# Kernel tuning notes

Hardware: AMD Instinct MI355X
Metric: run time of the kernel (lower is better)

Reference implementation:

```python
import jax, jax.numpy as jnp
import numpy as np

V, E, H = 100000, 300, 256          # pretrained vectors, emb_dim, rep_dim
B, QLEN, DOC, S = 32, 32, 2048, 64  # batch, max_query_len, max_doc_len, max_num_sent
L = DOC // S                        # sentence length (lengths sum exactly to DOC)
VOCAB = V + 2                       # + extra token + padding idx


def _uniform(k, shape, scale):
    return jax.random.uniform(k, shape, jnp.float32, -scale, scale)


def setup_inputs() -> dict:
    key = jax.random.key(0)
    ks = jax.random.split(key, 16)
    s = 1.0 / np.sqrt(H)  # PyTorch GRU default init scale
    return {
        "queries": jax.random.randint(ks[0], (B, QLEN), 0, V),
        "query_lengths": jax.random.randint(ks[1], (B,), QLEN // 2, QLEN + 1).astype(jnp.int32),
        "docs": jax.random.randint(ks[2], (B, DOC), 0, V),
        "sentence_lengths": jnp.full((B, S), L, dtype=jnp.int32),
        "emb": jax.random.normal(ks[3], (VOCAB, E), jnp.float32) * 0.1,
        "q_wih": _uniform(ks[4], (3 * H, E), s), "q_whh": _uniform(ks[5], (3 * H, H), s),
        "q_bih": _uniform(ks[6], (3 * H,), s), "q_bhh": _uniform(ks[7], (3 * H,), s),
        "f_wih": _uniform(ks[8], (3 * H, E), s), "f_whh": _uniform(ks[9], (3 * H, H), s),
        "f_bih": _uniform(ks[10], (3 * H,), s), "f_bhh": _uniform(ks[11], (3 * H,), s),
        "b_wih": _uniform(ks[12], (3 * H, E), s), "b_whh": _uniform(ks[13], (3 * H, H), s),
        "b_bih": _uniform(ks[14], (3 * H,), s), "b_bhh": _uniform(ks[15], (3 * H,), s),
    }


def _gru(x, wih, whh, bih, bhh, reverse=False):
    # x: (B, T, E) -> hidden states (B, T, H); PyTorch GRU cell equations.
    xg = jnp.einsum('bte,ge->btg', x, wih) + bih  # (B, T, 3H) input projections

    def step(h, xt):
        gh = h @ whh.T + bhh
        ir, iz, inn = jnp.split(xt, 3, axis=-1)
        hr, hz, hn = jnp.split(gh, 3, axis=-1)
        r = jax.nn.sigmoid(ir + hr)
        z = jax.nn.sigmoid(iz + hz)
        n = jnp.tanh(inn + r * hn)
        hnew = (1.0 - z) * n + z * h
        return hnew, hnew

    h0 = jnp.zeros((x.shape[0], whh.shape[1]), x.dtype)
    _, hs = jax.lax.scan(step, h0, jnp.swapaxes(xg, 0, 1), reverse=reverse)
    return jnp.swapaxes(hs, 0, 1)


def reference(queries, query_lengths, docs, sentence_lengths, emb,
              q_wih, q_whh, q_bih, q_bhh,
              f_wih, f_whh, f_bih, f_bhh,
              b_wih, b_whh, b_bih, b_bhh):
    q_emb = emb[queries]  # (B, QLEN, E)
    d_emb = emb[docs]     # (B, DOC, E)

    # Ragged per-sentence mean pooling (_get_facts) as one segment-mean per doc.
    def seg_mean(xb, lens):
        ids = jnp.repeat(jnp.arange(S), lens, total_repeat_length=DOC)
        sums = jax.ops.segment_sum(xb, ids, num_segments=S)
        return sums / jnp.maximum(lens, 1)[:, None].astype(xb.dtype)

    facts = jax.vmap(seg_mean)(d_emb, sentence_lengths)  # (B, S, E)

    # Question GRU: hidden state at the last valid token (pack_padded semantics).
    q_hs = _gru(q_emb, q_wih, q_whh, q_bih, q_bhh)
    q_rep = q_hs[jnp.arange(B), query_lengths - 1][:, None, :]  # (B, 1, H)

    # Input fusion: bidirectional GRU over facts, fwd + bwd halves summed (dropout off / eval).
    f_out = (_gru(facts, f_wih, f_whh, f_bih, f_bhh)
             + _gru(facts, b_wih, b_whh, b_bih, b_bhh, reverse=True))  # (B, S, H)

    num_facts = jnp.sum(sentence_lengths > 0, axis=1)
    return q_rep, f_out, num_facts
```

## Files before the change

### kernel.cpp

```cpp
#include <hip/hip_runtime.h>

#define Bn   32
#define QL   32
#define DOCn 2048
#define Sn   64
#define En   300
#define Hn   256

typedef short bf16x8 __attribute__((ext_vector_type(8)));
typedef short s16x4  __attribute__((ext_vector_type(4)));
typedef float f32x4  __attribute__((ext_vector_type(4)));

static __device__ __forceinline__ float b2f(short s){
  unsigned int u = ((unsigned int)(unsigned short)s) << 16;
  float f; __builtin_memcpy(&f, &u, 4); return f;
}
static __device__ __forceinline__ short f2b(float f){
  unsigned int u; __builtin_memcpy(&u, &f, 4);
  u = u + 0x7fffu + ((u >> 16) & 1u);
  return (short)(u >> 16);
}
static __device__ __forceinline__ float sigm(float x){ return 1.0f/(1.0f+__expf(-x)); }
static __device__ __forceinline__ float tanhx(float x){ return 1.0f - 2.0f/(__expf(2.0f*x)+1.0f); }
static __device__ __forceinline__ f32x4 mfma16(bf16x8 a, bf16x8 b, f32x4 c){
  return __builtin_amdgcn_mfma_f32_16x16x32_bf16(a, b, c, 0, 0, 0);
}
static __device__ __forceinline__ void bar_lgkm(){
  asm volatile("s_waitcnt lgkmcnt(0)\n\ts_barrier" ::: "memory");
}

__global__ __launch_bounds__(256) void k_facts(
    const int* __restrict__ docs, const int* __restrict__ slens,
    const float* __restrict__ emb,
    const float* __restrict__ f_wih, const float* __restrict__ b_wih,
    const float* __restrict__ q_wih,
    short* __restrict__ facts, short* __restrict__ wcvt,
    float* __restrict__ dout)
{
  const int tid = threadIdx.x;

  if (blockIdx.x >= 2048){
    const int rg0 = (blockIdx.x - 2048)*8;
#pragma unroll
    for (int rr = 0; rr < 8; ++rr){
      const int rg = rg0 + rr;
      const int z = rg / 768, g = rg % 768;
      const float* src = ((z == 0) ? f_wih : (z == 1) ? b_wih : q_wih) + (long)g*En;
      short* dst = wcvt + (long)rg*320;
      for (int c = tid; c < 320; c += 256)
        dst[c] = (c < En) ? f2b(src[c]) : (short)0;
    }
    return;
  }

  __shared__ int pref[2*Sn];
  const int blk = blockIdx.x;
  const int b = blk >> 6, s = blk & 63;
  if (tid < Sn){
    const int v = slens[b*Sn + tid];
    int x = v;
#pragma unroll
    for (int d = 1; d < 64; d <<= 1){
      const int y = __shfl_up(x, d, 64);
      if (tid >= d) x += y;
    }
    pref[tid] = x - v;
    pref[Sn + tid] = v;
    if (s == 0){
      const unsigned long long m = __ballot(v > 0);
      if (tid == 0) dout[Bn*Hn + (long)Bn*Sn*Hn + b] = (float)__popcll(m);
    }
  }
  __syncthreads();
  const int off = pref[s];
  const int len = pref[Sn + s];
  const int e0 = tid;
  float a0 = 0.f, a1 = 0.f;
  const int* dtok = docs + b*DOCn + off;
  int tk = (len > 0) ? dtok[0] : 0;
  for (int l = 0; l < len; ++l){
    const int tkn = (l + 1 < len) ? dtok[l+1] : 0;
    const float* row = emb + (long)tk*En;
    a0 += row[e0];
    if (e0 + 256 < En) a1 += row[e0+256];
    tk = tkn;
  }
  const float inv = 1.0f / (float)(len > 0 ? len : 1);
  short* frow = facts + ((long)b*Sn + s)*320;
  frow[e0] = f2b(a0*inv);
  if (e0 < 64) frow[e0+256] = (e0 + 256 < En) ? f2b(a1*inv) : (short)0;
}

__global__ __launch_bounds__(256) void k_xg(
    const short* __restrict__ facts, const short* __restrict__ wcvt,
    const int* __restrict__ queries, const float* __restrict__ emb,
    const float* __restrict__ q_bih, const float* __restrict__ q_bhh,
    const float* __restrict__ f_bih, const float* __restrict__ f_bhh,
    const float* __restrict__ b_bih, const float* __restrict__ b_bhh,
    short* __restrict__ q_xgi, short* __restrict__ f_xgi,
    short* __restrict__ b_xgi)
{
  const int z = blockIdx.z;
  const int bm = blockIdx.x, bn = blockIdx.y;
  const bool isq = (z == 2);
  if (isq && bm >= 8) return;

  const float* bih = (z == 0) ? f_bih : (z == 1) ? b_bih : q_bih;
  const float* bhh = (z == 0) ? f_bhh : (z == 1) ? b_bhh : q_bhh;
  short*       xgi = (z == 0) ? f_xgi : (z == 1) ? b_xgi : q_xgi;

  __shared__ alignas(16) short Al[2][128][40];
  const int tid = threadIdx.x;
  const int l = tid & 63, w = tid >> 6;
  const int wm = w & 1, wn = w >> 1;
  const int l15 = l & 15, lq = l >> 4;
  const int ak8 = w*8;

  bf16x8 bfr[2][10];
#pragma unroll
  for (int nt = 0; nt < 2; ++nt){
    const int g = bn*64 + wn*32 + nt*16 + l15;
    const short* wr = wcvt + ((long)z*768 + g)*320;
#pragma unroll
    for (int kk = 0; kk < 10; ++kk)
      bfr[nt][kk] = *(const bf16x8*)&wr[kk*32 + lq*8];
  }

  const short* asrc_f0 = nullptr; const short* asrc_f1 = nullptr;
  const float* asrc_q0 = nullptr; const float* asrc_q1 = nullptr;
  if (isq){
    asrc_q0 = emb + (long)queries[bm*128 + l]*En;
    asrc_q1 = emb + (long)queries[bm*128 + 64 + l]*En;
  } else {
    asrc_f0 = facts + (long)(bm*128 + l)*320;
    asrc_f1 = facts + (long)(bm*128 + 64 + l)*320;
  }

  bf16x8 va0, va1;
#define LDA_(KK) do{ const int k0_ = (KK)*32 + ak8; \
    if (!isq){ \
      va0 = *(const bf16x8*)(asrc_f0 + k0_); \
      va1 = *(const bf16x8*)(asrc_f1 + k0_); \
    } else if (k0_ + 7 < En){ \
      const f32x4 p0 = *(const f32x4*)(asrc_q0+k0_), p1 = *(const f32x4*)(asrc_q0+k0_+4); \
      const f32x4 p2 = *(const f32x4*)(asrc_q1+k0_), p3 = *(const f32x4*)(asrc_q1+k0_+4); \
      _Pragma("unroll") for (int j = 0; j < 4; ++j){ \
        va0[j] = f2b(p0[j]); va0[4+j] = f2b(p1[j]); \
        va1[j] = f2b(p2[j]); va1[4+j] = f2b(p3[j]); } \
    } else { \
      _Pragma("unroll") for (int j = 0; j < 8; ++j){ const int k_ = k0_ + j; \
        va0[j] = (k_ < En) ? f2b(asrc_q0[k_]) : (short)0; \
        va1[j] = (k_ < En) ? f2b(asrc_q1[k_]) : (short)0; } \
    } }while(0)
#define STA_(BUF) do{ *(bf16x8*)&Al[BUF][l][ak8] = va0; \
    *(bf16x8*)&Al[BUF][64 + l][ak8] = va1; }while(0)

  LDA_(0); STA_(0);
  __syncthreads();

  f32x4 acc[4][2] = {};
#pragma unroll
  for (int kk = 0; kk < 10; ++kk){
    if (kk < 9) LDA_(kk+1);
#pragma unroll
    for (int mt = 0; mt < 4; ++mt){
      bf16x8 a = *(const bf16x8*)&Al[kk&1][wm*64 + mt*16 + l15][lq*8];
      acc[mt][0] = mfma16(a, bfr[0][kk], acc[mt][0]);
      acc[mt][1] = mfma16(a, bfr[1][kk], acc[mt][1]);
    }
    if (kk < 9) STA_((kk+1)&1);
    __syncthreads();
  }
#undef LDA_
#undef STA_

#pragma unroll
  for (int nt = 0; nt < 2; ++nt){
    const int cg = bn*64 + wn*32 + nt*16 + l15;
    float bias = bih[cg];
    if (cg < 512) bias += bhh[cg];
    const int gate = cg >> 8, hc = cg & 255;
#pragma unroll
    for (int mt = 0; mt < 4; ++mt){
      const int r0 = bm*128 + wm*64 + mt*16 + lq*4;
#pragma unroll
      for (int p = 0; p < 4; ++p){
        const int r = r0 + p;
        const int row = isq ? ((r & 31)*32 + (r >> 5)) : ((r & 63)*32 + (r >> 6));
        xgi[(long)row*1024 + hc*4 + gate] = f2b(acc[mt][nt][p] + bias);
      }
    }
  }
}

__global__ __launch_bounds__(1024) void k_gru(
    const short* __restrict__ q_xg, const short* __restrict__ f_xg,
    const short* __restrict__ b_xg,
    const float* __restrict__ q_whh, const float* __restrict__ q_bhh,
    const float* __restrict__ f_whh, const float* __restrict__ f_bhh,
    const float* __restrict__ b_whh, const float* __restrict__ b_bhh,
    const int* __restrict__ qlens,
    float* __restrict__ dout)
{
  __shared__ alignas(16) short hl[2*16*264];
  __shared__ alignas(16) short wl[7*1024*8];

  const int gru = blockIdx.x >> 1;
  const int mh  = blockIdx.x & 1;
  const int tid = threadIdx.x;
  const int l = tid & 63, w = tid >> 6;
  const int l15 = l & 15, lq = l >> 4;

  const float* whh = (gru == 0) ? q_whh : (gru == 1) ? f_whh : b_whh;
  const float* bhh = (gru == 0) ? q_bhh : (gru == 1) ? f_bhh : b_bhh;
  const short* xgp = (gru == 0) ? q_xg  : (gru == 1) ? f_xg  : b_xg;
  const int T = (gru == 0) ? QL : Sn;

  const int c = w*16 + l15;

  bf16x8 wf[3][6];
  float bhn = 0.f;
#pragma unroll
  for (int gi = 0; gi < 3; ++gi){
    const int g = gi*256 + c;
    const float* wr = whh + (long)g*Hn;
#pragma unroll
    for (int kk = 0; kk < 8; ++kk){
      const f32x4 f0 = *(const f32x4*)(wr + kk*32 + lq*8);
      const f32x4 f1 = *(const f32x4*)(wr + kk*32 + lq*8 + 4);
      bf16x8 v;
#pragma unroll
      for (int j = 0; j < 4; ++j){ v[j] = f2b(f0[j]); v[4+j] = f2b(f1[j]); }
      if (kk < 5 || (kk == 5 && gi < 2)) wf[gi][kk] = v;
      else if (kk == 5)                  *(bf16x8*)&wl[(6*1024 + tid)*8] = v;
      else                               *(bf16x8*)&wl[(((kk-6)*3 + gi)*1024 + tid)*8] = v;
    }
    if (gi == 2) bhn = bhh[g];
  }

  float hreg[4] = {};
  int qlen_m[4];
#pragma unroll
  for (int p = 0; p < 4; ++p) qlen_m[p] = (gru == 0) ? qlens[mh*16 + lq*4 + p] : -1;

  const int vo = (mh*16 + lq*4)*1024 + c*4;
  float* qdst  = dout + (mh*16 + lq*4)*Hn + c;
  float* fbase = dout + Bn*Hn + (long)(mh*16 + lq*4)*(Sn*Hn) + c;

  s16x4 preA[4], preB[4];

#define TOF(TT) ((gru == 2) ? (T - 1 - (TT)) : (TT))
#define LOADP(PRE, TI) do{ const short* sb_ = xgp + (long)(TI)*32768 + vo; \
    PRE[0] = *(const s16x4*)(sb_); \
    PRE[1] = *(const s16x4*)(sb_ + 1024); \
    PRE[2] = *(const s16x4*)(sb_ + 2048); \
    PRE[3] = *(const s16x4*)(sb_ + 3072); }while(0)

#define GRU_STEP(TT, DOM, HIN, HOUT, PRE) do{ \
    f32x4 acc0 = (f32x4){0.f,0.f,0.f,0.f}; \
    f32x4 acc1 = (f32x4){0.f,0.f,0.f,0.f}; \
    f32x4 acc2 = (f32x4){bhn,bhn,bhn,bhn}; \
    if (DOM){ \
      _Pragma("unroll") for (int kk = 0; kk < 5; ++kk){ \
        const bf16x8 a = *(const bf16x8*)&(HIN)[l15*264 + kk*32 + lq*8]; \
        acc0 = mfma16(a, wf[0][kk], acc0); \
        acc1 = mfma16(a, wf[1][kk], acc1); \
        acc2 = mfma16(a, wf[2][kk], acc2); \
      } \
      { const bf16x8 a = *(const bf16x8*)&(HIN)[l15*264 + 5*32 + lq*8]; \
        const bf16x8 w2 = *(const bf16x8*)&wl[(6*1024 + tid)*8]; \
        acc0 = mfma16(a, wf[0][5], acc0); \
        acc1 = mfma16(a, wf[1][5], acc1); \
        acc2 = mfma16(a, w2, acc2); } \
      { const bf16x8 a = *(const bf16x8*)&(HIN)[l15*264 + 6*32 + lq*8]; \
        const bf16x8 w0 = *(const bf16x8*)&wl[(0*1024 + tid)*8]; \
        const bf16x8 w1 = *(const bf16x8*)&wl[(1*1024 + tid)*8]; \
        const bf16x8 w2 = *(const bf16x8*)&wl[(2*1024 + tid)*8]; \
        acc0 = mfma16(a, w0, acc0); \
        acc1 = mfma16(a, w1, acc1); \
        acc2 = mfma16(a, w2, acc2); } \
      { const bf16x8 a = *(const bf16x8*)&(HIN)[l15*264 + 7*32 + lq*8]; \
        const bf16x8 w0 = *(const bf16x8*)&wl[(3*1024 + tid)*8]; \
        const bf16x8 w1 = *(const bf16x8*)&wl[(4*1024 + tid)*8]; \
        const bf16x8 w2 = *(const bf16x8*)&wl[(5*1024 + tid)*8]; \
        acc0 = mfma16(a, w0, acc0); \
        acc1 = mfma16(a, w1, acc1); \
        acc2 = mfma16(a, w2, acc2); } \
    } \
    const int t_ = TOF(TT); \
    _Pragma("unroll") for (int p = 0; p < 4; ++p){ \
      const float ir = b2f(PRE[p][0]), iz = b2f(PRE[p][1]), in_ = b2f(PRE[p][2]); \
      const float rr = sigm(ir + acc0[p]); \
      const float zz = sigm(iz + acc1[p]); \
      const float nn = tanhx(in_ + rr*acc2[p]); \
      const float hn = (1.0f - zz)*nn + zz*hreg[p]; \
      hreg[p] = hn; \
      (HOUT)[(lq*4 + p)*264 + c] = f2b(hn); \
      if (gru == 0){ if (t_ == qlen_m[p] - 1) qdst[p*Hn] = hn; } \
      else { atomicAdd(fbase + p*(Sn*Hn) + t_*Hn, hn); } \
    } \
  }while(0)

  short* h0 = hl;
  short* h1 = hl + 4224;

  LOADP(preA, TOF(0));
  LOADP(preB, TOF(1));
  __builtin_amdgcn_sched_barrier(0);
  GRU_STEP(0, 0, h1, h0, preA);
  bar_lgkm();
  LOADP(preA, TOF(2));
  __builtin_amdgcn_sched_barrier(0);
  GRU_STEP(1, 1, h0, h1, preB);
  bar_lgkm();

  for (int tt = 2; tt < T; tt += 2){
    const int tiB = (tt+1 < T) ? (tt+1) : (T-1);
    LOADP(preB, TOF(tiB));
    __builtin_amdgcn_sched_barrier(0);
    GRU_STEP(tt, 1, h1, h0, preA);
    bar_lgkm();
    const int tiA = (tt+2 < T) ? (tt+2) : (T-1);
    LOADP(preA, TOF(tiA));
    __builtin_amdgcn_sched_barrier(0);
    GRU_STEP(tt+1, 1, h0, h1, preB);
    bar_lgkm();
  }
#undef TOF
#undef LOADP
#undef GRU_STEP
}

extern "C" void kernel_launch(void* const* d_in, const int* in_sizes, int n_in,
                              void* d_out, int out_size, void* d_ws, size_t ws_size,
                              hipStream_t stream)
{
  const int*   queries = (const int*)d_in[0];
  const int*   qlens   = (const int*)d_in[1];
  const int*   docs    = (const int*)d_in[2];
  const int*   slens   = (const int*)d_in[3];
  const float* emb     = (const float*)d_in[4];
  const float* q_wih   = (const float*)d_in[5];
  const float* q_whh   = (const float*)d_in[6];
  const float* q_bih   = (const float*)d_in[7];
  const float* q_bhh   = (const float*)d_in[8];
  const float* f_wih   = (const float*)d_in[9];
  const float* f_whh   = (const float*)d_in[10];
  const float* f_bih   = (const float*)d_in[11];
  const float* f_bhh   = (const float*)d_in[12];
  const float* b_wih   = (const float*)d_in[13];
  const float* b_whh   = (const float*)d_in[14];
  const float* b_bih   = (const float*)d_in[15];
  const float* b_bhh   = (const float*)d_in[16];

  char* wsb = (char*)d_ws;
  short* f_xgi = (short*)(wsb);
  short* b_xgi = (short*)(wsb +  4194304);
  short* q_xgi = (short*)(wsb +  8388608);
  short* facts = (short*)(wsb + 10485760);
  short* wcvt  = (short*)(wsb + 11796480);

  float* dout = (float*)d_out;

  k_facts<<<dim3(2048 + 288), 256, 0, stream>>>(docs, slens, emb,
                                                f_wih, b_wih, q_wih,
                                                facts, wcvt, dout);
  k_xg   <<<dim3(16, 12, 3), 256, 0, stream>>>(facts, wcvt, queries, emb,
                                               q_bih, q_bhh, f_bih, f_bhh,
                                               b_bih, b_bhh,
                                               q_xgi, f_xgi, b_xgi);
  k_gru  <<<dim3(6), 1024, 0, stream>>>(q_xgi, f_xgi, b_xgi, q_whh, q_bhh,
                                        f_whh, f_bhh, b_whh, b_bhh,
                                        qlens, dout);
}
```

Baseline: 518.7 us.

## Repack input-gate projections per thread and vectorize fact embedding gather

Result: faster. 486.7 us (-6.2%).

```diff
diff --git a/kernel.cpp b/kernel.cpp
--- a/kernel.cpp
+++ b/kernel.cpp
@@ -74,21 +74,26 @@
   __syncthreads();
   const int off = pref[s];
   const int len = pref[Sn + s];
-  const int e0 = tid;
   float a0 = 0.f, a1 = 0.f;
   const int* dtok = docs + b*DOCn + off;
   int tk = (len > 0) ? dtok[0] : 0;
   for (int l = 0; l < len; ++l){
     const int tkn = (l + 1 < len) ? dtok[l+1] : 0;
-    const float* row = emb + (long)tk*En;
-    a0 += row[e0];
-    if (e0 + 256 < En) a1 += row[e0+256];
+    if (tid < 150){
+      const float2 v = *(const float2*)(emb + (long)tk*En + 2*tid);
+      a0 += v.x; a1 += v.y;
+    }
     tk = tkn;
   }
   const float inv = 1.0f / (float)(len > 0 ? len : 1);
   short* frow = facts + ((long)b*Sn + s)*320;
-  frow[e0] = f2b(a0*inv);
-  if (e0 < 64) frow[e0+256] = (e0 + 256 < En) ? f2b(a1*inv) : (short)0;
+  if (tid < 150){
+    frow[2*tid]   = f2b(a0*inv);
+    frow[2*tid+1] = f2b(a1*inv);
+  } else if (tid < 160){
+    const int e = tid - 150;
+    frow[300 + 2*e] = 0; frow[301 + 2*e] = 0;
+  }
 }
 
 __global__ __launch_bounds__(256) void k_xg(
@@ -180,14 +185,19 @@
     float bias = bih[cg];
     if (cg < 512) bias += bhh[cg];
     const int gate = cg >> 8, hc = cg & 255;
+    const int wslot = (hc >> 4)*64 + (hc & 15);
 #pragma unroll
     for (int mt = 0; mt < 4; ++mt){
       const int r0 = bm*128 + wm*64 + mt*16 + lq*4;
 #pragma unroll
       for (int p = 0; p < 4; ++p){
         const int r = r0 + p;
-        const int row = isq ? ((r & 31)*32 + (r >> 5)) : ((r & 63)*32 + (r >> 6));
-        xgi[(long)row*1024 + hc*4 + gate] = f2b(acc[mt][nt][p] + bias);
+        const int t_ = isq ? (r & 31) : (r & 63);
+        const int b_ = isq ? (r >> 5) : (r >> 6);
+        const int mh_ = b_ >> 4, rb = b_ & 15;
+        const long sidx = (long)t_*32768 + mh_*16384
+                        + (long)(wslot + (rb >> 2)*16)*16 + (rb & 3)*3 + gate;
+        xgi[sidx] = f2b(acc[mt][nt][p] + bias);
       }
     }
   }
@@ -243,20 +253,29 @@
 #pragma unroll
   for (int p = 0; p < 4; ++p) qlen_m[p] = (gru == 0) ? qlens[mh*16 + lq*4 + p] : -1;
 
-  const int vo = (mh*16 + lq*4)*1024 + c*4;
+  const int so = mh*16384 + tid*16;
   float* qdst  = dout + (mh*16 + lq*4)*Hn + c;
   float* fbase = dout + Bn*Hn + (long)(mh*16 + lq*4)*(Sn*Hn) + c;
 
-  s16x4 preA[4], preB[4];
+  bf16x8 preA0, preA1, preB0, preB1;
 
 #define TOF(TT) ((gru == 2) ? (T - 1 - (TT)) : (TT))
-#define LOADP(PRE, TI) do{ const short* sb_ = xgp + (long)(TI)*32768 + vo; \
-    PRE[0] = *(const s16x4*)(sb_); \
-    PRE[1] = *(const s16x4*)(sb_ + 1024); \
-    PRE[2] = *(const s16x4*)(sb_ + 2048); \
-    PRE[3] = *(const s16x4*)(sb_ + 3072); }while(0)
-
-#define GRU_STEP(TT, DOM, HIN, HOUT, PRE) do{ \
+#define LOADP(P0, P1, TI) do{ const short* sb_ = xgp + (long)(TI)*32768 + so; \
+    P0 = *(const bf16x8*)(sb_); P1 = *(const bf16x8*)(sb_ + 8); }while(0)
+
+#define GRU_EW(P, HOUT, IRV, IZV, INV) do{ \
+      const float ir = b2f(IRV), iz = b2f(IZV), in_ = b2f(INV); \
+      const float rr = sigm(ir + acc0[P]); \
+      const float zz = sigm(iz + acc1[P]); \
+      const float nn = tanhx(in_ + rr*acc2[P]); \
+      const float hn = (1.0f - zz)*nn + zz*hreg[P]; \
+      hreg[P] = hn; \
+      (HOUT)[(lq*4 + P)*264 + c] = f2b(hn); \
+      if (gru == 0){ if (t_ == qlen_m[P] - 1) qdst[P*Hn] = hn; } \
+      else { atomicAdd(fbase + P*(Sn*Hn) + t_*Hn, hn); } \
+    }while(0)
+
+#define GRU_STEP(TT, DOM, HIN, HOUT, PR0, PR1) do{ \
     f32x4 acc0 = (f32x4){0.f,0.f,0.f,0.f}; \
     f32x4 acc1 = (f32x4){0.f,0.f,0.f,0.f}; \
     f32x4 acc2 = (f32x4){bhn,bhn,bhn,bhn}; \
@@ -288,46 +307,40 @@
         acc2 = mfma16(a, w2, acc2); } \
     } \
     const int t_ = TOF(TT); \
-    _Pragma("unroll") for (int p = 0; p < 4; ++p){ \
-      const float ir = b2f(PRE[p][0]), iz = b2f(PRE[p][1]), in_ = b2f(PRE[p][2]); \
-      const float rr = sigm(ir + acc0[p]); \
-      const float zz = sigm(iz + acc1[p]); \
-      const float nn = tanhx(in_ + rr*acc2[p]); \
-      const float hn = (1.0f - zz)*nn + zz*hreg[p]; \
-      hreg[p] = hn; \
-      (HOUT)[(lq*4 + p)*264 + c] = f2b(hn); \
-      if (gru == 0){ if (t_ == qlen_m[p] - 1) qdst[p*Hn] = hn; } \
-      else { atomicAdd(fbase + p*(Sn*Hn) + t_*Hn, hn); } \
-    } \
+    GRU_EW(0, HOUT, PR0[0], PR0[1], PR0[2]); \
+    GRU_EW(1, HOUT, PR0[3], PR0[4], PR0[5]); \
+    GRU_EW(2, HOUT, PR0[6], PR0[7], PR1[0]); \
+    GRU_EW(3, HOUT, PR1[1], PR1[2], PR1[3]); \
   }while(0)
 
   short* h0 = hl;
   short* h1 = hl + 4224;
 
-  LOADP(preA, TOF(0));
-  LOADP(preB, TOF(1));
+  LOADP(preA0, preA1, TOF(0));
+  LOADP(preB0, preB1, TOF(1));
   __builtin_amdgcn_sched_barrier(0);
-  GRU_STEP(0, 0, h1, h0, preA);
+  GRU_STEP(0, 0, h1, h0, preA0, preA1);
   bar_lgkm();
-  LOADP(preA, TOF(2));
+  LOADP(preA0, preA1, TOF(2));
   __builtin_amdgcn_sched_barrier(0);
-  GRU_STEP(1, 1, h0, h1, preB);
+  GRU_STEP(1, 1, h0, h1, preB0, preB1);
   bar_lgkm();
 
   for (int tt = 2; tt < T; tt += 2){
     const int tiB = (tt+1 < T) ? (tt+1) : (T-1);
-    LOADP(preB, TOF(tiB));
+    LOADP(preB0, preB1, TOF(tiB));
     __builtin_amdgcn_sched_barrier(0);
-    GRU_STEP(tt, 1, h1, h0, preA);
+    GRU_STEP(tt, 1, h1, h0, preA0, preA1);
     bar_lgkm();
     const int tiA = (tt+2 < T) ? (tt+2) : (T-1);
-    LOADP(preA, TOF(tiA));
+    LOADP(preA0, preA1, TOF(tiA));
     __builtin_amdgcn_sched_barrier(0);
-    GRU_STEP(tt+1, 1, h0, h1, preB);
+    GRU_STEP(tt+1, 1, h0, h1, preB0, preB1);
     bar_lgkm();
   }
 #undef TOF
 #undef LOADP
+#undef GRU_EW
 #undef GRU_STEP
 }
 
```
